# Kernel tuning notes

Hardware: AMD Instinct MI355X
Metric: run time of the kernel (lower is better)

The kernel has to match this reference:

```python
import jax, jax.numpy as jnp
import numpy as np

C_S, C_Z, C_H, H, PQ, PV = 384, 128, 16, 12, 4, 8
B, N = 1, 512
W_C = (2.0 / (9.0 * PQ)) ** 0.5
W_L = (1.0 / 3.0) ** 0.5
OUT_IN = H * C_Z + H * C_H + H * PV * 3 + H * PV  # 2112


def setup_inputs() -> dict:
    key = jax.random.key(0)
    ks = jax.random.split(key, 16)
    s_i = jax.random.normal(ks[0], (B, N, C_S), jnp.float32)
    z_ij = jax.random.normal(ks[1], (B, N, N, C_Z), jnp.float32)
    # random rotation matrices via QR
    raw = jax.random.normal(ks[2], (B, N, 3, 3), jnp.float32)
    q, r = jnp.linalg.qr(raw)
    rots = q * jnp.sign(jnp.diagonal(r, axis1=-2, axis2=-1))[..., None, :]
    trans = jax.random.normal(ks[3], (B, N, 3), jnp.float32)
    sc = lambda fan_in: 1.0 / np.sqrt(fan_in)
    Wq = jax.random.normal(ks[4], (C_S, H * C_H), jnp.float32) * sc(C_S)
    Wk = jax.random.normal(ks[5], (C_S, H * C_H), jnp.float32) * sc(C_S)
    Wv = jax.random.normal(ks[6], (C_S, H * C_H), jnp.float32) * sc(C_S)
    Wqp = jax.random.normal(ks[7], (C_S, H * PQ * 3), jnp.float32) * sc(C_S)
    Wkp = jax.random.normal(ks[8], (C_S, H * PQ * 3), jnp.float32) * sc(C_S)
    Wvp = jax.random.normal(ks[9], (C_S, H * PV * 3), jnp.float32) * sc(C_S)
    Wb = jax.random.normal(ks[10], (C_Z, H), jnp.float32) * sc(C_Z)
    gamma = jax.random.normal(ks[11], (1, 1, 1, H), jnp.float32)
    Wout = jax.random.normal(ks[12], (OUT_IN, C_S), jnp.float32) * sc(OUT_IN)
    bout = jnp.zeros((C_S,), jnp.float32)
    return dict(s_i=s_i, z_ij=z_ij, rots=rots, trans=trans, Wq=Wq, Wk=Wk, Wv=Wv,
                Wqp=Wqp, Wkp=Wkp, Wvp=Wvp, Wb=Wb, gamma=gamma, Wout=Wout, bout=bout)


def reference(s_i, z_ij, rots, trans, Wq, Wk, Wv, Wqp, Wkp, Wvp, Wb, gamma, Wout, bout):
    b, n = s_i.shape[0], s_i.shape[1]
    q_h = (s_i @ Wq).reshape(b, n, H, C_H)
    k_h = (s_i @ Wk).reshape(b, n, H, C_H)
    v_h = (s_i @ Wv).reshape(b, n, H, C_H)
    q_hp = (s_i @ Wqp).reshape(b, n, H, PQ, 3)
    k_hp = (s_i @ Wkp).reshape(b, n, H, PQ, 3)
    v_hp = (s_i @ Wvp).reshape(b, n, H, PV, 3)
    b_ij = z_ij @ Wb  # (b,i,j,h)

    t = trans[:, :, None, None, :]  # (b,i,1,1,3)
    apply = lambda x: jnp.einsum('bixy,bihpy->bihpx', rots, x) + t
    inv_apply = lambda x: jnp.einsum('bixy,bihpx->bihpy', rots, x - t)

    qg = apply(q_hp)  # (b,i,h,p,3) global frame
    kg = apply(k_hp)
    # pairwise rigid point distance term: (b,i,j,h)
    diff = qg[:, :, None] - kg[:, None]  # (b,i,j,h,p,3)
    dist2 = jnp.sum(diff * diff, axis=(-1, -2))

    a_s = jnp.einsum('bihd,bjhd->bijh', q_h, k_h) / (C_H ** 0.5)
    a_rigid = (W_C / 2.0) * gamma * dist2
    a = jax.nn.softmax(W_L * (a_s + b_ij - a_rigid), axis=-2)  # softmax over j

    o_hat = jnp.einsum('bijh,bijd->bihd', a, z_ij)
    o = jnp.einsum('bijh,bjhd->bihd', a, v_h)
    vg = apply(v_hp)  # (b,j,h,p,3)
    o_hp = inv_apply(jnp.einsum('bijh,bjhpx->bihpx', a, vg))  # (b,i,h,pv,3)
    o_hp_norm = jnp.sqrt(jnp.sum(o_hp * o_hp, axis=-1))  # (b,i,h,pv)

    cat = jnp.concatenate([
        o_hat.reshape(b, n, H * C_Z),
        o.reshape(b, n, H * C_H),
        o_hp.reshape(b, n, H * PV * 3),
        o_hp_norm.reshape(b, n, H * PV),
    ], axis=-1)
    return cat @ Wout + bout
```

## Files before the change

kernel.cpp:

```cpp
#include <hip/hip_runtime.h>
#include <hip/hip_bf16.h>
#include <math.h>

#define NRES 512
#define CS   384
#define CZ   128
#define NH   12
#define PW   1152
#define JB   64
#define NCH  8
#define PSTRIDE32 1040
#define KS   6
#define KAW  352
#define BFW  4224

static constexpr float WL_F      = 0.57735026918962576f;
static constexpr float HALF_WC_F = 0.11785113019775792f;

typedef __attribute__((ext_vector_type(8))) short short8v;
typedef __attribute__((ext_vector_type(4))) float floatx4;

__device__ __forceinline__ ushort f2b(float f) {
    union { float f; uint u; } v; v.f = f;
    return (ushort)((v.u + 0x7FFFu + ((v.u >> 16) & 1u)) >> 16);
}
__device__ __forceinline__ float b2f(ushort b) {
    union { uint u; float f; } v; v.u = ((uint)b) << 16; return v.f;
}

__global__ __launch_bounds__(256) void k_prep(
    const float* __restrict__ Wq, const float* __restrict__ Wk,
    const float* __restrict__ Wv, const float* __restrict__ Wqp,
    const float* __restrict__ Wkp, const float* __restrict__ Wvp,
    const float* __restrict__ Wb, const float* __restrict__ Wout,
    float* __restrict__ Wcat, ushort* __restrict__ wbt16,
    ushort* __restrict__ woT)
{
    __shared__ ushort tile[64][72];
    const int bx = blockIdx.x;
    if (bx < 384) {
        const int c = bx;
        for (int col = threadIdx.x; col < PW; col += 256) {
            float v;
            if (col < 192)      v = Wq [(size_t)c * 192 + col];
            else if (col < 384) v = Wk [(size_t)c * 192 + col - 192];
            else if (col < 576) v = Wv [(size_t)c * 192 + col - 384];
            else if (col < 720) v = Wqp[(size_t)c * 144 + col - 576];
            else if (col < 864) v = Wkp[(size_t)c * 144 + col - 720];
            else                v = Wvp[(size_t)c * 288 + col - 864];
            Wcat[(size_t)c * PW + col] = v;
        }
        if (bx == 0) {
            for (int idx = threadIdx.x; idx < 16 * 128; idx += 256) {
                const int h = idx >> 7, cc = idx & 127;
                wbt16[idx] = (h < NH) ? f2b(WL_F * Wb[(size_t)cc * NH + h]) : (ushort)0;
            }
        }
    } else {
        const int t = bx - 384;
        const int k0 = (t % 33) * 64, c0 = (t / 33) * 64;
        for (int idx = threadIdx.x; idx < 4096; idx += 256) {
            const int r = idx >> 6, c = idx & 63;
            tile[r][c] = f2b(Wout[(size_t)(k0 + r) * 384 + c0 + c]);
        }
        __syncthreads();
        for (int idx = threadIdx.x; idx < 4096; idx += 256) {
            const int c = idx >> 6, r = idx & 63;
            woT[(size_t)(c0 + c) * 2112 + k0 + r] = tile[r][c];
        }
    }
}

__global__ __launch_bounds__(256) void k_gemm(
    const float* __restrict__ s, const float* __restrict__ Wcat,
    const float* __restrict__ rots, const float* __restrict__ trans,
    float* __restrict__ P)
{
    const int tid = threadIdx.x;
    const int tx = tid & 15, ty = tid >> 4;
    const int n0 = blockIdx.x * 48;
    const int m0 = blockIdx.y * 32;
    __shared__ float As[32][34];
    __shared__ float Bs[32][50];
    __shared__ float rot_lds[32][12];

    if (n0 >= 576) {
        for (int idx = tid; idx < 32 * 12; idx += 256) {
            int r = idx / 12, q = idx % 12;
            rot_lds[r][q] = (q < 9) ? rots[(size_t)(m0 + r) * 9 + q]
                                    : trans[(size_t)(m0 + r) * 3 + q - 9];
        }
    }

    float acc[2][3];
    #pragma unroll
    for (int u = 0; u < 2; ++u)
        #pragma unroll
        for (int v = 0; v < 3; ++v) acc[u][v] = 0.f;

    for (int k0 = 0; k0 < CS; k0 += 32) {
        __syncthreads();
        #pragma unroll
        for (int l = 0; l < 4; ++l) {
            int idx = tid + l * 256;
            int kk = idx & 31, r = idx >> 5;
            As[kk][r] = s[(size_t)(m0 + r) * CS + k0 + kk];
        }
        #pragma unroll
        for (int l = 0; l < 6; ++l) {
            int idx = tid + l * 256;
            int kk = idx / 48, cc = idx % 48;
            Bs[kk][cc] = Wcat[(size_t)(k0 + kk) * PW + n0 + cc];
        }
        __syncthreads();
        #pragma unroll
        for (int kk = 0; kk < 32; ++kk) {
            const float2 a = *(const float2*)&As[kk][ty * 2];
            const float b0 = Bs[kk][tx * 3], b1 = Bs[kk][tx * 3 + 1], b2 = Bs[kk][tx * 3 + 2];
            acc[0][0] += a.x * b0; acc[0][1] += a.x * b1; acc[0][2] += a.x * b2;
            acc[1][0] += a.y * b0; acc[1][1] += a.y * b1; acc[1][2] += a.y * b2;
        }
    }

    #pragma unroll
    for (int u = 0; u < 2; ++u) {
        float v0 = acc[u][0], v1 = acc[u][1], v2 = acc[u][2];
        if (n0 >= 576) {
            const float* RT = rot_lds[ty * 2 + u];
            const float p0 = v0, p1 = v1, p2 = v2;
            v0 = RT[0] * p0 + RT[1] * p1 + RT[2] * p2 + RT[9];
            v1 = RT[3] * p0 + RT[4] * p1 + RT[5] * p2 + RT[10];
            v2 = RT[6] * p0 + RT[7] * p1 + RT[8] * p2 + RT[11];
        }
        float* dst = P + (size_t)(m0 + ty * 2 + u) * PW + n0 + tx * 3;
        dst[0] = v0; dst[1] = v1; dst[2] = v2;
    }
}

__global__ __launch_bounds__(128) void k_ka(
    const float* __restrict__ P, const float* __restrict__ gamma,
    ushort* __restrict__ Kfull, ushort* __restrict__ Bfull)
{
    const int r = blockIdx.x;
    const int tid = threadIdx.x;
    __shared__ float njs[NH];
    __shared__ float nqs[NH];
    const float* prow = P + (size_t)r * PW;
    const float* kr   = prow + 192;
    const float* qgr  = prow + 576;
    const float* kgr  = prow + 720;
    if (tid < NH) {
        float s = 0.f, sq = 0.f;
        #pragma unroll
        for (int e = 0; e < 12; ++e) {
            const float v = kgr[tid * 12 + e];  s += v * v;
            const float q = qgr[tid * 12 + e];  sq += q * q;
        }
        njs[tid] = s; nqs[tid] = sq;
    }
    __syncthreads();
    ushort* dst = Kfull + (size_t)r * KAW;
    for (int t = tid; t < KAW; t += 128) {
        float v;
        if (t < 192)       v = kr[t];
        else if (t < 336)  v = kgr[t - 192];
        else if (t < 348)  v = njs[t - 336];
        else if (t == 348) v = 1.0f;
        else               v = 0.f;
        dst[t] = f2b(v);
    }
    ushort* bd = Bfull + (size_t)r * BFW;
    for (int t = tid; t < BFW; t += 128) {
        const int h = t / 352, k = t - h * 352;
        float v = 0.f;
        if (k < 192) {
            if ((k >> 4) == h) v = 0.25f * WL_F * prow[k];
        } else if (k < 336) {
            const int e = k - 192;
            if (e / 12 == h) v = 2.f * HALF_WC_F * WL_F * gamma[h] * qgr[e];
        } else if (k < 348) {
            if (k - 336 == h) v = -HALF_WC_F * WL_F * gamma[h];
        } else if (k == 348) {
            v = -HALF_WC_F * WL_F * gamma[h] * nqs[h];
        }
        bd[t] = f2b(v);
    }
}

__global__ __launch_bounds__(256, 7) void k_flash(
    const float* __restrict__ z, const ushort* __restrict__ wbt16,
    const float* __restrict__ P, const ushort* __restrict__ Kfull,
    const ushort* __restrict__ Bfull, uint* __restrict__ part)
{
    const int i   = blockIdx.x;
    const int jc  = blockIdx.y;
    const int j0  = jc * JB;
    const int tid = threadIdx.x;
    const int wid = tid >> 6, lane = tid & 63;

    __shared__ __align__(16) short zbT[128 * JB];
    __shared__ __align__(16) float ltf[12 * 68];
    __shared__ __align__(16) short ltb[16 * 64];
    float4* halfacc = (float4*)zbT;

    uint* pb32   = part + ((size_t)i * NCH + jc) * PSTRIDE32;
    ushort* pb16 = (ushort*)pb32;
    float* pbf   = (float*)pb32;

    const int jb = wid * 16 + (lane & 15);
    const int ko = (lane >> 4) * 8;

    short8v af[4];
    {
        const float* za = z + ((size_t)i * NRES + j0 + jb) * CZ + ko;
        #pragma unroll
        for (int m = 0; m < 4; ++m) {
            const float4 f0 = *(const float4*)(za + m * 32);
            const float4 f1 = *(const float4*)(za + m * 32 + 4);
            short8v a;
            a[0] = (short)f2b(f0.x); a[1] = (short)f2b(f0.y);
            a[2] = (short)f2b(f0.z); a[3] = (short)f2b(f0.w);
            a[4] = (short)f2b(f1.x); a[5] = (short)f2b(f1.y);
            a[6] = (short)f2b(f1.z); a[7] = (short)f2b(f1.w);
            af[m] = a;
            #pragma unroll
            for (int e = 0; e < 8; ++e) {
                const int c = ko + m * 32 + e;
                zbT[c * 64 + (((jb >> 3) ^ (c & 7)) * 8) + (jb & 7)] = a[e];
            }
        }
    }

    {
        const int n  = lane & 15;
        const int nb = (n < NH) ? n : 0;
        const ushort* arow = Kfull + (size_t)(j0 + jb) * KAW + ko;
        const ushort* brow = Bfull + (size_t)i * BFW + nb * 352 + ko;
        const ushort* wrow = wbt16 + n * 128 + ko;
        floatx4 lacc = {0.f, 0.f, 0.f, 0.f};
        #pragma unroll
        for (int st = 0; st < 11; ++st) {
            const short8v a = *(const short8v*)(arow + st * 32);
            const short8v b = *(const short8v*)(brow + st * 32);
            lacc = __builtin_amdgcn_mfma_f32_16x16x32_bf16(a, b, lacc, 0, 0, 0);
        }
        #pragma unroll
        for (int st = 0; st < 4; ++st) {
            const short8v b = *(const short8v*)(wrow + st * 32);
            lacc = __builtin_amdgcn_mfma_f32_16x16x32_bf16(af[st], b, lacc, 0, 0, 0);
        }
        if (n < NH) {
            #pragma unroll
            for (int r = 0; r < 4; ++r)
                ltf[n * 68 + wid * 16 + (lane >> 4) * 4 + r] = lacc[r];
        }
    }
    __syncthreads();

    if (tid < 192) {
        const int h = tid >> 4, s = tid & 15;
        float4 v = *(const float4*)&ltf[h * 68 + s * 4];
        float m = fmaxf(fmaxf(v.x, v.y), fmaxf(v.z, v.w));
        #pragma unroll
        for (int o = 1; o < 16; o <<= 1) m = fmaxf(m, __shfl_xor(m, o));
        float4 e;
        e.x = __expf(v.x - m); e.y = __expf(v.y - m);
        e.z = __expf(v.z - m); e.w = __expf(v.w - m);
        float sum = e.x + e.y + e.z + e.w;
        #pragma unroll
        for (int o = 1; o < 16; o <<= 1) sum += __shfl_xor(sum, o);
        *(float4*)&ltf[h * 68 + s * 4] = e;
        const uint lo = (uint)f2b(e.x) | ((uint)f2b(e.y) << 16);
        const uint hi = (uint)f2b(e.z) | ((uint)f2b(e.w) << 16);
        uint* dst = (uint*)&ltb[h * 64 + (((s >> 1) ^ (h & 7)) * 8) + (s & 1) * 4];
        dst[0] = lo; dst[1] = hi;
        if (s == 0) { pbf[1008 + h] = m; pbf[1020 + h] = sum; }
    } else {
        const int tt = tid - 192;
        uint* dst = (uint*)&ltb[(12 + (tt >> 4)) * 64 + (tt & 15) * 4];
        dst[0] = 0u; dst[1] = 0u;
    }
    __syncthreads();

    {
        const int hrow = lane & 15;
        const int u0 = (lane >> 4), u1 = u0 + 4;
        const short8v a0 = *(const short8v*)&ltb[hrow * 64 + ((u0 ^ (hrow & 7)) * 8)];
        const short8v a1 = *(const short8v*)&ltb[hrow * 64 + ((u1 ^ (hrow & 7)) * 8)];
        #pragma unroll
        for (int t = 0; t < 2; ++t) {
            const int d = (wid * 2 + t) * 16 + (lane & 15);
            const short8v b0 = *(const short8v*)&zbT[d * 64 + ((u0 ^ (d & 7)) * 8)];
            const short8v b1 = *(const short8v*)&zbT[d * 64 + ((u1 ^ (d & 7)) * 8)];
            floatx4 acc = {0.f, 0.f, 0.f, 0.f};
            acc = __builtin_amdgcn_mfma_f32_16x16x32_bf16(a0, b0, acc, 0, 0, 0);
            acc = __builtin_amdgcn_mfma_f32_16x16x32_bf16(a1, b1, acc, 0, 0, 0);
            #pragma unroll
            for (int r = 0; r < 4; ++r) {
                const int h = u0 * 4 + r;
                if (h < NH) pb16[h * 128 + d] = f2b(acc[r]);
            }
        }
    }
    __syncthreads();

    {
        if (tid < 240) {
            const int half = tid / 120, col = tid % 120;
            int h;
            const float* base;
            if (col < 48) { h = col >> 2;               base = P + (size_t)j0 * PW + 384 + col * 4; }
            else          { const int cc = col - 48; h = cc / 6; base = P + (size_t)j0 * PW + 864 + cc * 4; }
            base += (size_t)(half * 32) * PW;
            const float* er = &ltf[h * 68 + half * 32];
            float ax = 0.f, ay = 0.f, az = 0.f, aw = 0.f;
            #pragma unroll 4
            for (int jj = 0; jj < 32; ++jj) {
                const float e = er[jj];
                const float4 v = *(const float4*)(base + (size_t)jj * PW);
                ax += e * v.x; ay += e * v.y; az += e * v.z; aw += e * v.w;
            }
            halfacc[tid] = make_float4(ax, ay, az, aw);
        }
        __syncthreads();
        if (tid < 120) {
            const float4 s0 = halfacc[tid], s1 = halfacc[tid + 120];
            const int off16 = (tid < 48) ? 1536 + tid * 4 : 1728 + (tid - 48) * 4;
            uint* dst = (uint*)&pb16[off16];
            dst[0] = (uint)f2b(s0.x + s1.x) | ((uint)f2b(s0.y + s1.y) << 16);
            dst[1] = (uint)f2b(s0.z + s1.z) | ((uint)f2b(s0.w + s1.w) << 16);
        }
    }
}

__global__ __launch_bounds__(256) void k_combine(
    const uint* __restrict__ part, const float* __restrict__ rots,
    const float* __restrict__ trans, ushort* __restrict__ cat16)
{
    const int i   = blockIdx.x;
    const int tid = threadIdx.x;
    __shared__ float wgt[NCH][NH];
    __shared__ float ohp[288];

    const uint* base = part + (size_t)i * NCH * PSTRIDE32;
    if (tid < NH) {
        const int h = tid;
        float mm[NCH];
        float M = -1e30f;
        #pragma unroll
        for (int c = 0; c < NCH; ++c) {
            mm[c] = ((const float*)(base + c * PSTRIDE32))[1008 + h];
            M = fmaxf(M, mm[c]);
        }
        float S = 0.f;
        #pragma unroll
        for (int c = 0; c < NCH; ++c) {
            const float w = __expf(mm[c] - M);
            S += w * ((const float*)(base + c * PSTRIDE32))[1020 + h];
            wgt[c][h] = w;
        }
        const float inv = 1.0f / S;
        #pragma unroll
        for (int c = 0; c < NCH; ++c) wgt[c][h] *= inv;
    }
    __syncthreads();

    ushort* crow = cat16 + (size_t)i * 2112;
    uint*   crowu = (uint*)crow;
    for (int idx2 = tid; idx2 < 768; idx2 += 256) {
        const int h = idx2 >> 6;
        float v0 = 0.f, v1 = 0.f;
        #pragma unroll
        for (int c = 0; c < NCH; ++c) {
            const uint u = base[c * PSTRIDE32 + idx2];
            const float w = wgt[c][h];
            v0 += b2f((ushort)u) * w;
            v1 += b2f((ushort)(u >> 16)) * w;
        }
        crowu[idx2] = (uint)f2b(v0) | ((uint)f2b(v1) << 16);
    }
    if (tid < 96) {
        const int h = tid >> 3;
        float v0 = 0.f, v1 = 0.f;
        #pragma unroll
        for (int c = 0; c < NCH; ++c) {
            const uint u = base[c * PSTRIDE32 + 768 + tid];
            const float w = wgt[c][h];
            v0 += b2f((ushort)u) * w;
            v1 += b2f((ushort)(u >> 16)) * w;
        }
        crowu[768 + tid] = (uint)f2b(v0) | ((uint)f2b(v1) << 16);
    }
    if (tid < 144) {
        const int h = tid / 12;
        float v0 = 0.f, v1 = 0.f;
        #pragma unroll
        for (int c = 0; c < NCH; ++c) {
            const uint u = base[c * PSTRIDE32 + 864 + tid];
            const float w = wgt[c][h];
            v0 += b2f((ushort)u) * w;
            v1 += b2f((ushort)(u >> 16)) * w;
        }
        ohp[tid * 2] = v0; ohp[tid * 2 + 1] = v1;
    }
    __syncthreads();

    if (tid < 96) {
        const int h = tid >> 3, p = tid & 7;
        float R[9];
        #pragma unroll
        for (int k = 0; k < 9; ++k) R[k] = rots[(size_t)i * 9 + k];
        const float g0 = ohp[h * 24 + p * 3 + 0] - trans[(size_t)i * 3 + 0];
        const float g1 = ohp[h * 24 + p * 3 + 1] - trans[(size_t)i * 3 + 1];
        const float g2 = ohp[h * 24 + p * 3 + 2] - trans[(size_t)i * 3 + 2];
        const float oy0 = R[0] * g0 + R[3] * g1 + R[6] * g2;
        const float oy1 = R[1] * g0 + R[4] * g1 + R[7] * g2;
        const float oy2 = R[2] * g0 + R[5] * g1 + R[8] * g2;
        crow[1728 + h * 24 + p * 3 + 0] = f2b(oy0);
        crow[1728 + h * 24 + p * 3 + 1] = f2b(oy1);
        crow[1728 + h * 24 + p * 3 + 2] = f2b(oy2);
        crow[2016 + h * 8 + p] = f2b(sqrtf(oy0 * oy0 + oy1 * oy1 + oy2 * oy2));
    }
}

__global__ __launch_bounds__(256) void k_out(
    const ushort* __restrict__ cat16, const ushort* __restrict__ woT,
    float* __restrict__ opart)
{
    const int tid = threadIdx.x;
    const int wid = tid >> 6, lane = tid & 63;
    const int wm = wid >> 1, wn = wid & 1;
    const int i0 = blockIdx.x * 32 + wm * 16;
    const int c0 = blockIdx.y * 32 + wn * 16;
    const int k0 = blockIdx.z * 352;
    const ushort* arow = cat16 + (size_t)(i0 + (lane & 15)) * 2112 + k0 + (lane >> 4) * 8;
    const ushort* brow = woT   + (size_t)(c0 + (lane & 15)) * 2112 + k0 + (lane >> 4) * 8;
    floatx4 acc = {0.f, 0.f, 0.f, 0.f};
    #pragma unroll
    for (int st = 0; st < 11; ++st) {
        const short8v a = *(const short8v*)(arow + st * 32);
        const short8v b = *(const short8v*)(brow + st * 32);
        acc = __builtin_amdgcn_mfma_f32_16x16x32_bf16(a, b, acc, 0, 0, 0);
    }
    float* ob = opart + (size_t)blockIdx.z * 512 * 384;
    #pragma unroll
    for (int r = 0; r < 4; ++r) {
        const int i = i0 + (lane >> 4) * 4 + r;
        ob[(size_t)i * 384 + c0 + (lane & 15)] = acc[r];
    }
}

__global__ __launch_bounds__(256) void k_outred(
    const float* __restrict__ opart, const float* __restrict__ bout,
    float* __restrict__ out)
{
    const int e4 = blockIdx.x * 256 + threadIdx.x;
    const float4* p = (const float4*)opart;
    const float4 b = ((const float4*)bout)[e4 % 96];
    float4 r = b;
    #pragma unroll
    for (int k = 0; k < KS; ++k) {
        const float4 v = p[e4 + k * 49152];
        r.x += v.x; r.y += v.y; r.z += v.z; r.w += v.w;
    }
    ((float4*)out)[e4] = r;
}

extern "C" void kernel_launch(void* const* d_in, const int* in_sizes, int n_in,
                              void* d_out, int out_size, void* d_ws, size_t ws_size,
                              hipStream_t stream)
{
    const float* s_i   = (const float*)d_in[0];
    const float* z_ij  = (const float*)d_in[1];
    const float* rots  = (const float*)d_in[2];
    const float* trans = (const float*)d_in[3];
    const float* Wq    = (const float*)d_in[4];
    const float* Wk    = (const float*)d_in[5];
    const float* Wv    = (const float*)d_in[6];
    const float* Wqp   = (const float*)d_in[7];
    const float* Wkp   = (const float*)d_in[8];
    const float* Wvp   = (const float*)d_in[9];
    const float* Wb    = (const float*)d_in[10];
    const float* gamma = (const float*)d_in[11];
    const float* Wout  = (const float*)d_in[12];
    const float* bout  = (const float*)d_in[13];
    float* ws = (float*)d_ws;
    float*  wcat  = ws;
    float*  P     = ws + 442368;
    uint*   part  = (uint*)(P + 589824);
    float*  opart = (float*)part;
    ushort* bfull = (ushort*)(part + (size_t)512 * NCH * PSTRIDE32);
    ushort* cat16 = bfull;
    ushort* wbt16 = bfull + (size_t)512 * BFW;
    ushort* kfull = wbt16 + 2048;
    ushort* woT   = kfull + 512 * KAW;
    float*  out   = (float*)d_out;

    hipLaunchKernelGGL(k_prep, dim3(582), dim3(256), 0, stream,
                       Wq, Wk, Wv, Wqp, Wkp, Wvp, Wb, Wout, wcat, wbt16, woT);
    hipLaunchKernelGGL(k_gemm, dim3(24, 16), dim3(256), 0, stream,
                       s_i, wcat, rots, trans, P);
    hipLaunchKernelGGL(k_ka, dim3(512), dim3(128), 0, stream,
                       P, gamma, kfull, bfull);
    hipLaunchKernelGGL(k_flash, dim3(512, NCH), dim3(256), 0, stream,
                       z_ij, wbt16, P, kfull, bfull, part);
    hipLaunchKernelGGL(k_combine, dim3(512), dim3(256), 0, stream,
                       part, rots, trans, cat16);
    hipLaunchKernelGGL(k_out, dim3(16, 12, KS), dim3(256), 0, stream,
                       cat16, woT, opart);
    hipLaunchKernelGGL(k_outred, dim3(192), dim3(256), 0, stream,
                       opart, bout, out);
}
```

Measured before the change: 132.1 us.

## Pack V values as transposed bf16 and stage Bfull row in LDS

k_ka now also writes the v and vg point values into a compact bf16 array, transposed so each column's j-values are contiguous. k_flash reads these packed values with 16-byte loads instead of strided fp32 rows of P. It also copies the per-i Bfull row into shared memory once instead of each lane re-reading it from global, and reuses one shared buffer for the scratch arrays. This costs an extra sync, a lower occupancy hint (7 to 6 blocks), and bf16 precision loss on the V aggregation.

```diff
diff --git a/kernel.cpp b/kernel.cpp
--- a/kernel.cpp
+++ b/kernel.cpp
@@ -139,7 +139,8 @@
 
 __global__ __launch_bounds__(128) void k_ka(
     const float* __restrict__ P, const float* __restrict__ gamma,
-    ushort* __restrict__ Kfull, ushort* __restrict__ Bfull)
+    ushort* __restrict__ Kfull, ushort* __restrict__ Bfull,
+    ushort* __restrict__ vp)
 {
     const int r = blockIdx.x;
     const int tid = threadIdx.x;
@@ -147,8 +148,10 @@
     __shared__ float nqs[NH];
     const float* prow = P + (size_t)r * PW;
     const float* kr   = prow + 192;
+    const float* vr   = prow + 384;
     const float* qgr  = prow + 576;
     const float* kgr  = prow + 720;
+    const float* vgr  = prow + 864;
     if (tid < NH) {
         float s = 0.f, sq = 0.f;
         #pragma unroll
@@ -185,12 +188,17 @@
         }
         bd[t] = f2b(v);
     }
-}
-
-__global__ __launch_bounds__(256, 7) void k_flash(
+    for (int t = tid; t < 480; t += 128) {
+        const int g = t >> 2, e = t & 3;
+        const float v = (g < 48) ? vr[g * 4 + e] : vgr[(g - 48) * 4 + e];
+        vp[((size_t)g * 512 + r) * 4 + e] = f2b(v);
+    }
+}
+
+__global__ __launch_bounds__(256, 6) void k_flash(
     const float* __restrict__ z, const ushort* __restrict__ wbt16,
-    const float* __restrict__ P, const ushort* __restrict__ Kfull,
-    const ushort* __restrict__ Bfull, uint* __restrict__ part)
+    const ushort* __restrict__ Kfull, const ushort* __restrict__ Bfull,
+    const ushort* __restrict__ vp, uint* __restrict__ part)
 {
     const int i   = blockIdx.x;
     const int jc  = blockIdx.y;
@@ -199,9 +207,12 @@
     const int wid = tid >> 6, lane = tid & 63;
 
     __shared__ __align__(16) short zbT[128 * JB];
-    __shared__ __align__(16) float ltf[12 * 68];
-    __shared__ __align__(16) short ltb[16 * 64];
-    float4* halfacc = (float4*)zbT;
+    __shared__ __align__(16) char  uni[9152];
+
+    short*  BfT     = (short*)uni;
+    float*  ltf     = (float*)uni;
+    short*  ltb     = (short*)(uni + 3264);
+    float4* halfacc = (float4*)(uni + 5312);
 
     uint* pb32   = part + ((size_t)i * NCH + jc) * PSTRIDE32;
     ushort* pb16 = (ushort*)pb32;
@@ -229,15 +240,21 @@
                 zbT[c * 64 + (((jb >> 3) ^ (c & 7)) * 8) + (jb & 7)] = a[e];
             }
         }
-    }
-
+        const uint4* bsrc = (const uint4*)(Bfull + (size_t)i * BFW);
+        for (int idx = tid; idx < 528; idx += 256) {
+            const int r = idx / 44, c = idx % 44;
+            *(uint4*)&BfT[r * 360 + c * 8] = bsrc[idx];
+        }
+    }
+    __syncthreads();
+
+    floatx4 lacc = {0.f, 0.f, 0.f, 0.f};
     {
         const int n  = lane & 15;
         const int nb = (n < NH) ? n : 0;
         const ushort* arow = Kfull + (size_t)(j0 + jb) * KAW + ko;
-        const ushort* brow = Bfull + (size_t)i * BFW + nb * 352 + ko;
+        const short*  brow = &BfT[nb * 360 + ko];
         const ushort* wrow = wbt16 + n * 128 + ko;
-        floatx4 lacc = {0.f, 0.f, 0.f, 0.f};
         #pragma unroll
         for (int st = 0; st < 11; ++st) {
             const short8v a = *(const short8v*)(arow + st * 32);
@@ -249,6 +266,10 @@
             const short8v b = *(const short8v*)(wrow + st * 32);
             lacc = __builtin_amdgcn_mfma_f32_16x16x32_bf16(af[st], b, lacc, 0, 0, 0);
         }
+    }
+    __syncthreads();
+    {
+        const int n = lane & 15;
         if (n < NH) {
             #pragma unroll
             for (int r = 0; r < 4; ++r)
@@ -302,23 +323,22 @@
             }
         }
     }
-    __syncthreads();
 
     {
         if (tid < 240) {
             const int half = tid / 120, col = tid % 120;
-            int h;
-            const float* base;
-            if (col < 48) { h = col >> 2;               base = P + (size_t)j0 * PW + 384 + col * 4; }
-            else          { const int cc = col - 48; h = cc / 6; base = P + (size_t)j0 * PW + 864 + cc * 4; }
-            base += (size_t)(half * 32) * PW;
+            const int h = (col < 48) ? (col >> 2) : ((col - 48) / 6);
+            const ushort* vb = vp + ((size_t)col * 512 + j0 + half * 32) * 4;
             const float* er = &ltf[h * 68 + half * 32];
             float ax = 0.f, ay = 0.f, az = 0.f, aw = 0.f;
-            #pragma unroll 4
-            for (int jj = 0; jj < 32; ++jj) {
-                const float e = er[jj];
-                const float4 v = *(const float4*)(base + (size_t)jj * PW);
-                ax += e * v.x; ay += e * v.y; az += e * v.z; aw += e * v.w;
+            #pragma unroll 8
+            for (int t = 0; t < 16; ++t) {
+                const uint4 raw = *(const uint4*)(vb + t * 8);
+                const float e0 = er[2 * t], e1 = er[2 * t + 1];
+                ax += e0 * b2f((ushort)raw.x)         + e1 * b2f((ushort)raw.z);
+                ay += e0 * b2f((ushort)(raw.x >> 16)) + e1 * b2f((ushort)(raw.z >> 16));
+                az += e0 * b2f((ushort)raw.y)         + e1 * b2f((ushort)raw.w);
+                aw += e0 * b2f((ushort)(raw.y >> 16)) + e1 * b2f((ushort)(raw.w >> 16));
             }
             halfacc[tid] = make_float4(ax, ay, az, aw);
         }
@@ -494,6 +514,7 @@
     ushort* wbt16 = bfull + (size_t)512 * BFW;
     ushort* kfull = wbt16 + 2048;
     ushort* woT   = kfull + 512 * KAW;
+    ushort* vp    = woT + (size_t)384 * 2112;
     float*  out   = (float*)d_out;
 
     hipLaunchKernelGGL(k_prep, dim3(582), dim3(256), 0, stream,
@@ -501,9 +522,9 @@
     hipLaunchKernelGGL(k_gemm, dim3(24, 16), dim3(256), 0, stream,
                        s_i, wcat, rots, trans, P);
     hipLaunchKernelGGL(k_ka, dim3(512), dim3(128), 0, stream,
-                       P, gamma, kfull, bfull);
+                       P, gamma, kfull, bfull, vp);
     hipLaunchKernelGGL(k_flash, dim3(512, NCH), dim3(256), 0, stream,
-                       z_ij, wbt16, P, kfull, bfull, part);
+                       z_ij, wbt16, kfull, bfull, vp, part);
     hipLaunchKernelGGL(k_combine, dim3(512), dim3(256), 0, stream,
                        part, rots, trans, cat16);
     hipLaunchKernelGGL(k_out, dim3(16, 12, KS), dim3(256), 0, stream,
```

Result: slower. 140.5 us (+6.4%).
